# Optimization experiments

Measured on AMD Instinct MI355X. Metric: run time of the kernel, lower is better.

Reference implementation:

```python
import jax, jax.numpy as jnp
import numpy as np

B, C, N, V, W = 2, 4, 224, 7, 256
EMB, H = 256, 4
TOKEN_DIM = C * N           # 896
HF = int(C * 2.66)          # 10 (GDFN hidden features)
EPS_LN = 1e-6


def _dwconv3(x, w):
    # depthwise 3x3, padding=1; x:[B,Ch,Hh,Ww], w:[Ch,1,3,3]
    return jax.lax.conv_general_dilated(
        x, w, window_strides=(1, 1), padding='SAME',
        feature_group_count=x.shape[1],
        dimension_numbers=('NCHW', 'OIHW', 'NCHW'))


def _layernorm_c(x, g, b):
    # LayerNorm over channel dim (NCHW), eps=1e-6
    m = jnp.mean(x, axis=1, keepdims=True)
    v = jnp.mean((x - m) ** 2, axis=1, keepdims=True)
    return (x - m) / jnp.sqrt(v + EPS_LN) * g[None, :, None, None] + b[None, :, None, None]


def setup_inputs() -> dict:
    key = jax.random.key(0)
    ks = jax.random.split(key, 12)
    s = 0.02
    return {
        'buffer':     jax.random.normal(ks[0], (B, C, N, V, W), jnp.float32),
        'w_in':       jax.random.normal(ks[1], (EMB, TOKEN_DIM), jnp.float32) * s,
        'temperature': jnp.ones((1, H, 1, 1), jnp.float32),
        'ln1_g':      jnp.ones((EMB,), jnp.float32),
        'ln1_b':      jnp.zeros((EMB,), jnp.float32),
        'w_qkv':      jax.random.normal(ks[2], (3 * EMB, EMB), jnp.float32) * s,
        'w_qkv_dw':   jax.random.normal(ks[3], (3 * EMB, 1, 3, 3), jnp.float32) * s,
        'w_proj':     jax.random.normal(ks[4], (TOKEN_DIM, EMB), jnp.float32) * s,
        'w_attca':    jax.random.normal(ks[5], (2 * H, H), jnp.float32) * s,
        'ln2_g':      jnp.ones((C,), jnp.float32),
        'ln2_b':      jnp.zeros((C,), jnp.float32),
        'w_pin':      jax.random.normal(ks[6], (2 * HF, C), jnp.float32) * s,
        'w_dw':       jax.random.normal(ks[7], (2 * HF, 1, 3, 3), jnp.float32) * s,
        'w_pout':     jax.random.normal(ks[8], (C, HF), jnp.float32) * s,
    }


def reference(buffer, w_in, temperature, ln1_g, ln1_b, w_qkv, w_qkv_dw,
              w_proj, w_attca, ln2_g, ln2_b, w_pin, w_dw, w_pout):
    S = V * W
    d = EMB // H
    # b c n v w -> b (v w) (c n)
    x_tok = buffer.transpose(0, 3, 4, 1, 2).reshape(B, S, C * N)
    # b c n v w -> (b n) c v w
    x_res = buffer.transpose(0, 2, 1, 3, 4).reshape(B * N, C, V, W)

    x_tok = jnp.einsum('bsk,ek->bse', x_tok, w_in)                  # linear_in
    x = x_tok.reshape(B, V, W, EMB).transpose(0, 3, 1, 2)           # b emb v w
    x_norm = _layernorm_c(x, ln1_g, ln1_b)

    qkv = jnp.einsum('bchw,oc->bohw', x_norm, w_qkv)                # 1x1 conv
    qkv = _dwconv3(qkv, w_qkv_dw)
    q, k, v_ = jnp.split(qkv, 3, axis=1)

    def heads(t):  # b (h d) v w -> b h (v w) d
        return t.reshape(B, H, d, S).transpose(0, 1, 3, 2)
    q, k, v_ = heads(q), heads(k), heads(v_)

    # F.normalize(dim=-1), eps=1e-12
    q = q / jnp.maximum(jnp.linalg.norm(q, axis=-1, keepdims=True), 1e-12)
    k = k / jnp.maximum(jnp.linalg.norm(k, axis=-1, keepdims=True), 1e-12)

    attn_logits = jnp.einsum('bhid,bhjd->bhij', q, k) * temperature
    attn0 = jax.nn.softmax(attn_logits, axis=-1)
    attn1 = jnp.maximum(attn_logits, 0.0) ** 2
    attn1 = jax.nn.gelu(attn1, approximate=False) * attn1
    x_att = jnp.einsum('bhij,oh->boij', attn1, w_attca)             # 1x1 conv over heads
    scale, shift = jnp.split(x_att, 2, axis=1)
    attn = attn0 * (1.0 + scale) + shift

    out = jnp.einsum('bhij,bhjd->bhid', attn, v_)
    out = out.transpose(0, 1, 3, 2).reshape(B, EMB, V, W)           # b (h d) v w
    out = jnp.einsum('bchw,oc->bohw', out, w_proj)                  # proj to token_dim
    out = out.reshape(B, C, N, V, W).transpose(0, 2, 1, 3, 4).reshape(B * N, C, V, W)

    x2 = x_res + out
    epi = _layernorm_c(x2, ln2_g, ln2_b)
    # GDFN
    h_ = jnp.einsum('bchw,oc->bohw', epi, w_pin)
    h_ = _dwconv3(h_, w_dw)
    h1, h2 = jnp.split(h_, 2, axis=1)
    h_ = jax.nn.gelu(h1, approximate=False) * h2
    epi = jnp.einsum('bchw,oc->bohw', h_, w_pout)
    epi = x2 + epi

    return epi.reshape(B, N, C, V, W).transpose(0, 2, 1, 3, 4)      # b c n v w
```

## Files before the change

### kernel.cpp

```cpp
#include <hip/hip_runtime.h>
#include <math.h>

#define B_ 2
#define C_ 4
#define N_ 224
#define V_ 7
#define W_ 256
#define S_ 1792
#define EMB_ 256
#define H_ 4
#define D_ 64
#define TOK_ 896
#define HF_ 10
#define JC_ 4
#define JRANGE_ (S_ / JC_)
#define JSTEPS_ (JRANGE_ / 32)

typedef __attribute__((ext_vector_type(8))) short short8;
typedef __attribute__((ext_vector_type(4))) float f32x4;

#define MFMA16(a, b, c) __builtin_amdgcn_mfma_f32_16x16x32_bf16(a, b, c, 0, 0, 0)

__device__ inline short f2bf(float f) {
    union { float f; unsigned u; } x; x.f = f;
    unsigned u = x.u;
    unsigned r = (u + 0x7fffu + ((u >> 16) & 1u)) >> 16;
    return (short)r;
}
__device__ inline float bf2f(short s) {
    union { unsigned u; float f; } x;
    x.u = ((unsigned)(unsigned short)s) << 16;
    return x.f;
}

template<bool COLSUM, bool LNB, bool BBF>
__global__ __launch_bounds__(256) void gemm_kernel(
    const float* __restrict__ A, const void* __restrict__ Bv, float* __restrict__ Cm,
    int M, int N, int K, long b_bs, long c_bs,
    const float* __restrict__ csin, float* __restrict__ csout,
    const float* __restrict__ lg, const float* __restrict__ lb)
{
    const int bz = blockIdx.z;
    Cm += (long)bz * c_bs;
    const int m0 = blockIdx.y * 64, n0 = blockIdx.x * 128;
    __shared__ __align__(16) short As[64 * 32];
    __shared__ __align__(16) short Bs[128 * 32];
    const int t = threadIdx.x;
    const int lane = t & 63, wave = t >> 6;
    const int wr = wave >> 1, wc = wave & 1;
    const int col = lane & 15, grp = lane >> 4;
    const int arow = t >> 2, akc = (t & 3) * 8;
    const int bn = t & 127, bkc = (t >> 7) * 16;
    float mean = 0.f, rstd = 1.f;
    if (LNB) {
        float s = 0.f, q = 0.f;
        #pragma unroll
        for (int mb = 0; mb < 4; ++mb) {
            s += csin[((long)(bz * 4 + mb) * 2 + 0) * N + n0 + bn];
            q += csin[((long)(bz * 4 + mb) * 2 + 1) * N + n0 + bn];
        }
        mean = s * (1.f / 256.f);
        rstd = rsqrtf(q * (1.f / 256.f) - mean * mean + 1e-6f);
    }
    f32x4 acc[2][4];
    #pragma unroll
    for (int i = 0; i < 2; ++i)
        #pragma unroll
        for (int j = 0; j < 4; ++j) acc[i][j] = (f32x4){0.f, 0.f, 0.f, 0.f};
    for (int k0 = 0; k0 < K; k0 += 32) {
        {
            const float* ap = &A[(long)(m0 + arow) * K + k0 + akc];
            f32x4 a0 = *(const f32x4*)ap;
            f32x4 a1 = *(const f32x4*)(ap + 4);
            short8 av;
            av[0] = f2bf(a0[0]); av[1] = f2bf(a0[1]); av[2] = f2bf(a0[2]); av[3] = f2bf(a0[3]);
            av[4] = f2bf(a1[0]); av[5] = f2bf(a1[1]); av[6] = f2bf(a1[2]); av[7] = f2bf(a1[3]);
            int abyte = (arow << 6) + (akc << 1);
            *(short8*)((char*)As + (abyte ^ ((arow & 7) << 4))) = av;
        }
        {
            short8 b0, b1;
            if (BBF) {
                const short* Bp = (const short*)Bv + (long)bz * b_bs;
                #pragma unroll
                for (int j = 0; j < 8; ++j) {
                    b0[j] = Bp[(long)(k0 + bkc + j) * N + n0 + bn];
                    b1[j] = Bp[(long)(k0 + bkc + 8 + j) * N + n0 + bn];
                }
            } else {
                const float* Bp = (const float*)Bv + (long)bz * b_bs;
                #pragma unroll
                for (int j = 0; j < 16; ++j) {
                    float v = Bp[(long)(k0 + bkc + j) * N + n0 + bn];
                    if (LNB) v = fmaf((v - mean) * rstd, lg[k0 + bkc + j], lb[k0 + bkc + j]);
                    if (j < 8) b0[j] = f2bf(v); else b1[j - 8] = f2bf(v);
                }
            }
            int bbyte = (bn << 6) + (bkc << 1);
            *(short8*)((char*)Bs + ((bbyte) ^ ((bn & 7) << 4))) = b0;
            *(short8*)((char*)Bs + ((bbyte + 16) ^ ((bn & 7) << 4))) = b1;
        }
        __syncthreads();
        short8 af[2], bfv[4];
        #pragma unroll
        for (int mm = 0; mm < 2; ++mm) {
            int r = wr * 32 + mm * 16 + col;
            af[mm] = *(const short8*)((const char*)As + (((r << 6) + (grp << 4)) ^ ((r & 7) << 4)));
        }
        #pragma unroll
        for (int nn = 0; nn < 4; ++nn) {
            int r = wc * 64 + nn * 16 + col;
            bfv[nn] = *(const short8*)((const char*)Bs + (((r << 6) + (grp << 4)) ^ ((r & 7) << 4)));
        }
        #pragma unroll
        for (int mm = 0; mm < 2; ++mm)
            #pragma unroll
            for (int nn = 0; nn < 4; ++nn)
                acc[mm][nn] = MFMA16(af[mm], bfv[nn], acc[mm][nn]);
        __syncthreads();
    }
    #pragma unroll
    for (int mm = 0; mm < 2; ++mm)
        #pragma unroll
        for (int nn = 0; nn < 4; ++nn)
            #pragma unroll
            for (int r = 0; r < 4; ++r)
                Cm[(long)(m0 + wr * 32 + mm * 16 + grp * 4 + r) * N
                   + n0 + wc * 64 + nn * 16 + col] = acc[mm][nn][r];
    if (COLSUM) {
        float* red = (float*)As;
        #pragma unroll
        for (int nn = 0; nn < 4; ++nn) {
            float s = 0.f, q = 0.f;
            #pragma unroll
            for (int mm = 0; mm < 2; ++mm)
                #pragma unroll
                for (int r = 0; r < 4; ++r) { float v = acc[mm][nn][r]; s += v; q += v * v; }
            s += __shfl_xor(s, 16, 64); s += __shfl_xor(s, 32, 64);
            q += __shfl_xor(q, 16, 64); q += __shfl_xor(q, 32, 64);
            if (lane < 16) {
                int cidx = wc * 64 + nn * 16 + col;
                red[(wr * 128 + cidx) * 2]     = s;
                red[(wr * 128 + cidx) * 2 + 1] = q;
            }
        }
        __syncthreads();
        if (wave < 2 && lane < 16) {
            #pragma unroll
            for (int nn = 0; nn < 4; ++nn) {
                int cidx = wc * 64 + nn * 16 + col;
                float s = red[cidx * 2]     + red[(128 + cidx) * 2];
                float q = red[cidx * 2 + 1] + red[(128 + cidx) * 2 + 1];
                csout[((long)(bz * 4 + blockIdx.y) * 2 + 0) * N + n0 + cidx] = s;
                csout[((long)(bz * 4 + blockIdx.y) * 2 + 1) * N + n0 + cidx] = q;
            }
        }
    }
}

__global__ void dwconv3_kernel(const float* __restrict__ X, const float* __restrict__ Wt,
                               float* __restrict__ Y, short* __restrict__ vbf,
                               long total, int Ch)
{
    long idx = (long)blockIdx.x * blockDim.x + threadIdx.x;
    long stride = (long)gridDim.x * blockDim.x;
    for (; idx < total; idx += stride) {
        int w = (int)(idx % W_);
        long t = idx / W_;
        int h = (int)(t % V_); t /= V_;
        int ch = (int)(t % Ch);
        long img_ch = idx / ((long)V_ * W_);
        const float* wp = Wt + ch * 9;
        const float* xp = X + img_ch * (V_ * W_);
        float acc = 0.f;
        #pragma unroll
        for (int dy = -1; dy <= 1; ++dy) {
            int h2 = h + dy;
            if (h2 < 0 || h2 >= V_) continue;
            #pragma unroll
            for (int dx = -1; dx <= 1; ++dx) {
                int w2 = w + dx;
                if (w2 < 0 || w2 >= W_) continue;
                acc += xp[h2 * W_ + w2] * wp[(dy + 1) * 3 + (dx + 1)];
            }
        }
        Y[idx] = acc;
        if (vbf && ch >= 512) {
            int b = (int)(t / Ch);
            vbf[((long)b * 256 + (ch - 512)) * S_ + h * W_ + w] = f2bf(acc);
        }
    }
}

__global__ __launch_bounds__(256) void headnorm_kernel(
    const float* __restrict__ qkvd, const float* __restrict__ temp,
    short* __restrict__ qn, short* __restrict__ kn)
{
    int s0 = blockIdx.x * 64;
    int bh = blockIdx.y; int b = bh >> 2, h = bh & 3;
    int isq = blockIdx.z;
    int ch0 = b * 768 + (isq ? 0 : EMB_) + h * 64;
    short* dst = (isq ? qn : kn) + (long)bh * S_ * 64;
    __shared__ float tile[64][65];
    __shared__ float red[64][4];
    int t = threadIdx.x;
    int sl = t & 63, dg = t >> 6;
    float part = 0.f;
    for (int dd = 0; dd < 16; ++dd) {
        int d = dg * 16 + dd;
        float v = qkvd[(long)(ch0 + d) * S_ + s0 + sl];
        tile[sl][d] = v;
        part += v * v;
    }
    red[sl][dg] = part;
    __syncthreads();
    int d = t & 63, sg = t >> 6;
    float tmul = isq ? temp[h] : 1.f;
    for (int si = 0; si < 16; ++si) {
        int s = sg * 16 + si;
        float nrm = sqrtf(red[s][0] + red[s][1] + red[s][2] + red[s][3]);
        float scale = tmul / fmaxf(nrm, 1e-12f);
        dst[(long)(s0 + s) * 64 + d] = f2bf(tile[s][d] * scale);
    }
}

__global__ __launch_bounds__(256) void attn_kernel(
    const short* __restrict__ qn, const short* __restrict__ kn,
    const short* __restrict__ vbf, const float* __restrict__ wat,
    short* __restrict__ partY, float* __restrict__ partZ)
{
    const int h = threadIdx.x >> 6;
    const int lane = threadIdx.x & 63;
    const int col = lane & 15, grp = lane >> 4;
    const int itile = blockIdx.x;
    const int jc = blockIdx.y;
    const int b = blockIdx.z;
    const int ibase = itile * 16;
    const int bh = b * 4 + h;

    const short* qrow = qn + ((long)bh * S_ + ibase + col) * 64 + grp * 8;
    short8 qa0 = *(const short8*)qrow;
    short8 qa1 = *(const short8*)(qrow + 32);
    float wsc[4], wsh[4];
    #pragma unroll
    for (int hh = 0; hh < 4; ++hh) { wsc[hh] = wat[h * 4 + hh]; wsh[hh] = wat[(4 + h) * 4 + hh]; }

    __shared__ __align__(16) float exch[2][4][16][36];

    f32x4 y1[4], y2[4];
    #pragma unroll
    for (int dt = 0; dt < 4; ++dt) {
        y1[dt] = (f32x4){0.f, 0.f, 0.f, 0.f};
        y2[dt] = (f32x4){0.f, 0.f, 0.f, 0.f};
    }
    float z = 0.f;
    const short* kbase = kn + (long)bh * S_ * 64;
    const short* vbase = vbf + ((long)b * 256 + h * 64) * S_;
    const int joffA = (col & 3) + 8 * (col >> 2);

    for (int jt = 0; jt < JSTEPS_; ++jt) {
        const int jbase = jc * JRANGE_ + jt * 32;
        const int buf = jt & 1;
        f32x4 lf[2];
        __builtin_amdgcn_s_setprio(1);
        #pragma unroll
        for (int tt = 0; tt < 2; ++tt) {
            const short* krow = kbase + (long)(jbase + joffA + 4 * tt) * 64 + grp * 8;
            short8 ka0 = *(const short8*)krow;
            short8 ka1 = *(const short8*)(krow + 32);
            f32x4 a = (f32x4){0.f, 0.f, 0.f, 0.f};
            a = MFMA16(ka0, qa0, a);
            a = MFMA16(ka1, qa1, a);
            lf[tt] = a;
        }
        __builtin_amdgcn_s_setprio(0);
        f32x4 a1v[2];
        float ee[2][4];
        #pragma unroll
        for (int tt = 0; tt < 2; ++tt) {
            #pragma unroll
            for (int r = 0; r < 4; ++r) {
                float l = lf[tt][r];
                float rr = fmaxf(l, 0.f);
                float s1 = rr * rr;
                float u = fmaf(s1 * s1, 0.0713548162726f * s1, 1.59576912161f * s1);
                float sg = __builtin_amdgcn_rcpf(1.f + __expf(-u));
                a1v[tt][r] = s1 * sg * s1;
                ee[tt][r] = __expf(l);
            }
            *(f32x4*)&exch[buf][h][col][8 * grp + 4 * tt] = a1v[tt];
        }
        __syncthreads();
        short8 pa, pb;
        #pragma unroll
        for (int tt = 0; tt < 2; ++tt) {
            f32x4 scv = a1v[tt] * wsc[h];
            f32x4 shv = a1v[tt] * wsh[h];
            #pragma unroll
            for (int hh = 0; hh < 4; ++hh) {
                if (hh == h) continue;
                f32x4 o = *(const f32x4*)&exch[buf][hh][col][8 * grp + 4 * tt];
                scv += o * wsc[hh];
                shv += o * wsh[hh];
            }
            #pragma unroll
            for (int r = 0; r < 4; ++r) {
                float e = ee[tt][r];
                z += e;
                pa[tt * 4 + r] = f2bf(e * (1.f + scv[r]));
                pb[tt * 4 + r] = f2bf(shv[r]);
            }
        }
        __builtin_amdgcn_s_setprio(1);
        #pragma unroll
        for (int dt = 0; dt < 4; ++dt) {
            const short* vrow = vbase + (long)(dt * 16 + col) * S_ + jbase + grp * 8;
            short8 vb = *(const short8*)vrow;
            y1[dt] = MFMA16(pa, vb, y1[dt]);
            y2[dt] = MFMA16(pb, vb, y2[dt]);
        }
        __builtin_amdgcn_s_setprio(0);
    }

    z += __shfl_xor(z, 16, 64);
    z += __shfl_xor(z, 32, 64);
    if (grp == 0)
        partZ[((long)(jc * 2 + b) * 4 + h) * S_ + ibase + col] = z;

    float* tb = &exch[0][h][0][0];
    long ybase = ((((long)jc * 2 + b) * 4 + h) * 2) * 64 * S_;
    for (int acc = 0; acc < 2; ++acc) {
        #pragma unroll
        for (int dt = 0; dt < 4; ++dt) {
            f32x4 y = acc ? y2[dt] : y1[dt];
            #pragma unroll
            for (int r = 0; r < 4; ++r) tb[(grp * 4 + r) * 17 + col] = y[r];
            #pragma unroll
            for (int p = 0; p < 4; ++p) {
                float val = tb[col * 17 + p * 4 + grp];
                partY[ybase + ((long)acc * 64 + dt * 16 + p * 4 + grp) * S_ + ibase + col] = f2bf(val);
            }
        }
    }
}

__global__ __launch_bounds__(256) void combine_kernel(
    const short* __restrict__ partY, const float* __restrict__ partZ,
    short* __restrict__ outav)
{
    int idx = blockIdx.x * 256 + threadIdx.x;
    int i = idx % S_;
    int t = idx / S_;
    int d = t & 63; t >>= 6;
    int h = t & 3; int b = t >> 2;
    float y1 = 0.f, y2 = 0.f, z = 0.f;
    #pragma unroll
    for (int jc = 0; jc < JC_; ++jc) {
        long base = ((((long)jc * 2 + b) * 4 + h) * 2) * 64 * S_;
        y1 += bf2f(partY[base + (long)d * S_ + i]);
        y2 += bf2f(partY[base + (long)(64 + d) * S_ + i]);
        z  += partZ[((long)(jc * 2 + b) * 4 + h) * S_ + i];
    }
    outav[((long)b * 256 + h * 64 + d) * S_ + i] = f2bf(y1 / z + y2);
}

__global__ __launch_bounds__(256) void resid_pin_kernel(
    const float* __restrict__ buffer, const float* __restrict__ proj,
    const float* __restrict__ g2, const float* __restrict__ b2,
    const float* __restrict__ w_pin,
    float* __restrict__ x2, short* __restrict__ hbuf)
{
    int s = blockIdx.x * 256 + threadIdx.x;
    int bn = blockIdx.y;
    int b = bn / N_, n = bn % N_;
    float v[4];
    float sum = 0.f;
    #pragma unroll
    for (int c = 0; c < 4; ++c) {
        float xr = buffer[((long)(b * 4 + c) * N_ + n) * S_ + s];
        float pr = proj[((long)b * TOK_ + c * N_ + n) * S_ + s];
        v[c] = xr + pr;
        x2[((long)bn * 4 + c) * S_ + s] = v[c];
        sum += v[c];
    }
    float mean = sum * 0.25f;
    float var = 0.f;
    #pragma unroll
    for (int c = 0; c < 4; ++c) { float dd = v[c] - mean; var += dd * dd; }
    var *= 0.25f;
    float inv = rsqrtf(var + 1e-6f);
    float e[4];
    #pragma unroll
    for (int c = 0; c < 4; ++c) e[c] = (v[c] - mean) * inv * g2[c] + b2[c];
    for (int o = 0; o < 2 * HF_; ++o) {
        float a = 0.f;
        #pragma unroll
        for (int c = 0; c < 4; ++c) a += w_pin[o * 4 + c] * e[c];
        hbuf[((long)bn * (2 * HF_) + o) * S_ + s] = f2bf(a);
    }
}

__global__ __launch_bounds__(448) void gdfn_kernel(
    const short* __restrict__ hbuf, const float* __restrict__ w_dw,
    const float* __restrict__ w_pout, const float* __restrict__ x2,
    float* __restrict__ out)
{
    int xt = blockIdx.x;
    int bn = blockIdx.y;
    int b = bn / N_, n = bn % N_;
    int x0 = xt * 64;
    __shared__ float tile[20][7][66];
    int tid = threadIdx.x;
    for (int idx = tid; idx < 20 * 7 * 66; idx += 448) {
        int ch = idx / (7 * 66); int rem = idx % (7 * 66);
        int y = rem / 66; int xx = rem % 66;
        int gx = x0 + xx - 1;
        float v = 0.f;
        if (gx >= 0 && gx < W_) v = bf2f(hbuf[((long)bn * 20 + ch) * S_ + y * W_ + gx]);
        tile[ch][y][xx] = v;
    }
    __syncthreads();
    int y = tid / 64, x = tid & 63;
    float hd[20];
    #pragma unroll
    for (int ch = 0; ch < 20; ++ch) {
        const float* wp = w_dw + ch * 9;
        float acc = 0.f;
        #pragma unroll
        for (int dy = -1; dy <= 1; ++dy) {
            int yy = y + dy;
            if (yy < 0 || yy >= V_) continue;
            #pragma unroll
            for (int dx = -1; dx <= 1; ++dx)
                acc += tile[ch][yy][x + 1 + dx] * wp[(dy + 1) * 3 + (dx + 1)];
        }
        hd[ch] = acc;
    }
    float g[HF_];
    #pragma unroll
    for (int f = 0; f < HF_; ++f) {
        float h1 = hd[f];
        g[f] = 0.5f * h1 * (1.f + erff(h1 * 0.70710678118654752f)) * hd[HF_ + f];
    }
    int s = y * W_ + x0 + x;
    #pragma unroll
    for (int c = 0; c < 4; ++c) {
        float a = 0.f;
        #pragma unroll
        for (int f = 0; f < HF_; ++f) a += w_pout[c * HF_ + f] * g[f];
        out[((long)(b * 4 + c) * N_ + n) * S_ + s] = x2[((long)bn * 4 + c) * S_ + s] + a;
    }
}

extern "C" void kernel_launch(void* const* d_in, const int* in_sizes, int n_in,
                              void* d_out, int out_size, void* d_ws, size_t ws_size,
                              hipStream_t stream)
{
    const float* buffer = (const float*)d_in[0];
    const float* w_in   = (const float*)d_in[1];
    const float* temp   = (const float*)d_in[2];
    const float* ln1_g  = (const float*)d_in[3];
    const float* ln1_b  = (const float*)d_in[4];
    const float* w_qkv  = (const float*)d_in[5];
    const float* w_qkv_dw = (const float*)d_in[6];
    const float* w_proj = (const float*)d_in[7];
    const float* w_attca = (const float*)d_in[8];
    const float* ln2_g  = (const float*)d_in[9];
    const float* ln2_b  = (const float*)d_in[10];
    const float* w_pin  = (const float*)d_in[11];
    const float* w_dw   = (const float*)d_in[12];
    const float* w_pout = (const float*)d_in[13];
    float* out = (float*)d_out;

    float* ws = (float*)d_ws;
    float* qkvd    = ws;
    short* qn      = (short*)(ws + 2752512);
    short* kn      = (short*)(ws + 3211264);
    short* vbf     = (short*)(ws + 3670016);
    short* partY   = (short*)(ws + 4128768);
    float* partZ   = ws + 7798784;
    short* outav   = (short*)(ws + 7856128);
    float* xw      = ws + 8314880;
    float* colsum  = ws + 9232384;
    float* qkv     = ws + 9261056;
    float* outproj = ws + 12013568;
    float* x2      = ws + 15224832;
    short* hbuf    = (short*)(ws + 18436096);

    gemm_kernel<true, false, false><<<dim3(14, 4, 2), 256, 0, stream>>>(
        w_in, buffer, xw, EMB_, S_, TOK_, (long)TOK_ * S_, (long)EMB_ * S_,
        nullptr, colsum, nullptr, nullptr);

    gemm_kernel<false, true, false><<<dim3(14, 12, 2), 256, 0, stream>>>(
        w_qkv, xw, qkv, 3 * EMB_, S_, EMB_, (long)EMB_ * S_, (long)3 * EMB_ * S_,
        colsum, nullptr, ln1_g, ln1_b);

    {
        long total = (long)B_ * 3 * EMB_ * S_;
        dwconv3_kernel<<<(int)((total + 255) / 256), 256, 0, stream>>>(
            qkv, w_qkv_dw, qkvd, vbf, total, 3 * EMB_);
    }

    headnorm_kernel<<<dim3(28, 8, 2), 256, 0, stream>>>(qkvd, temp, qn, kn);

    attn_kernel<<<dim3(112, JC_, B_), 256, 0, stream>>>(qn, kn, vbf, w_attca, partY, partZ);

    combine_kernel<<<3584, 256, 0, stream>>>(partY, partZ, outav);

    gemm_kernel<false, false, true><<<dim3(14, 14, 2), 256, 0, stream>>>(
        w_proj, outav, outproj, TOK_, S_, EMB_, (long)EMB_ * S_, (long)TOK_ * S_,
        nullptr, nullptr, nullptr, nullptr);

    resid_pin_kernel<<<dim3(7, B_ * N_), 256, 0, stream>>>(
        buffer, outproj, ln2_g, ln2_b, w_pin, x2, hbuf);

    gdfn_kernel<<<dim3(4, B_ * N_), 448, 0, stream>>>(hbuf, w_dw, w_pout, x2, out);
}
```

Measured before the change: 217.2 us.

## Fuse dwconv into head-norm prep, fuse epilogue kernels, double attention j-splits

Merges the qkv depthwise conv with q/k L2 normalisation and the v bf16 conversion into one qkprep kernel, which removes the fp32 qkvd intermediate. It also merges the residual+LN2+pin and GDFN kernels into one epilogue that rebuilds x2 on the fly, dropping the x2 and hbuf buffers. Attention now uses twice as many j-chunks, and it swaps the double-buffered exchange and setprio hints for a single buffer with an extra barrier. The trade-offs are recomputed halo columns in the epilogue, more partial results to combine, and an extra __syncthreads on every attention step.

```diff
diff --git a/kernel.cpp b/kernel.cpp
--- a/kernel.cpp
+++ b/kernel.cpp
@@ -12,7 +12,7 @@
 #define D_ 64
 #define TOK_ 896
 #define HF_ 10
-#define JC_ 4
+#define JC_ 8
 #define JRANGE_ (S_ / JC_)
 #define JSTEPS_ (JRANGE_ / 32)
 
@@ -158,64 +158,61 @@
     }
 }
 
-__global__ void dwconv3_kernel(const float* __restrict__ X, const float* __restrict__ Wt,
-                               float* __restrict__ Y, short* __restrict__ vbf,
-                               long total, int Ch)
-{
-    long idx = (long)blockIdx.x * blockDim.x + threadIdx.x;
-    long stride = (long)gridDim.x * blockDim.x;
-    for (; idx < total; idx += stride) {
-        int w = (int)(idx % W_);
-        long t = idx / W_;
-        int h = (int)(t % V_); t /= V_;
-        int ch = (int)(t % Ch);
-        long img_ch = idx / ((long)V_ * W_);
-        const float* wp = Wt + ch * 9;
-        const float* xp = X + img_ch * (V_ * W_);
+__global__ __launch_bounds__(256) void qkprep_kernel(
+    const float* __restrict__ qkv, const float* __restrict__ temp,
+    const float* __restrict__ w_qkv_dw,
+    short* __restrict__ qn, short* __restrict__ kn, short* __restrict__ vbf)
+{
+    const int s0 = blockIdx.x * 64;
+    const int y  = s0 >> 8;
+    const int x0 = s0 & 255;
+    const int bh = blockIdx.y; const int b = bh >> 2, h = bh & 3;
+    const int mode = blockIdx.z;
+    const int wchbase = (mode == 0 ? 256 : (mode == 1 ? 0 : 512)) + h * 64;
+    const int chbase = b * 768 + wchbase;
+
+    int t = threadIdx.x;
+    int sl = t & 63, dg = t >> 6;
+    int x = x0 + sl;
+    float dval[16];
+    float part = 0.f;
+    #pragma unroll
+    for (int dd = 0; dd < 16; ++dd) {
+        int ch = dg * 16 + dd;
+        const float* xp = qkv + (long)(chbase + ch) * S_;
+        const float* wp = w_qkv_dw + (long)(wchbase + ch) * 9;
         float acc = 0.f;
         #pragma unroll
         for (int dy = -1; dy <= 1; ++dy) {
-            int h2 = h + dy;
-            if (h2 < 0 || h2 >= V_) continue;
+            int yy = y + dy;
+            if (yy < 0 || yy >= V_) continue;
+            const float* rp = xp + yy * W_;
             #pragma unroll
             for (int dx = -1; dx <= 1; ++dx) {
-                int w2 = w + dx;
-                if (w2 < 0 || w2 >= W_) continue;
-                acc += xp[h2 * W_ + w2] * wp[(dy + 1) * 3 + (dx + 1)];
-            }
-        }
-        Y[idx] = acc;
-        if (vbf && ch >= 512) {
-            int b = (int)(t / Ch);
-            vbf[((long)b * 256 + (ch - 512)) * S_ + h * W_ + w] = f2bf(acc);
-        }
-    }
-}
-
-__global__ __launch_bounds__(256) void headnorm_kernel(
-    const float* __restrict__ qkvd, const float* __restrict__ temp,
-    short* __restrict__ qn, short* __restrict__ kn)
-{
-    int s0 = blockIdx.x * 64;
-    int bh = blockIdx.y; int b = bh >> 2, h = bh & 3;
-    int isq = blockIdx.z;
-    int ch0 = b * 768 + (isq ? 0 : EMB_) + h * 64;
-    short* dst = (isq ? qn : kn) + (long)bh * S_ * 64;
+                int xx2 = x + dx;
+                if (xx2 < 0 || xx2 >= W_) continue;
+                acc += rp[xx2] * wp[(dy + 1) * 3 + dx + 1];
+            }
+        }
+        dval[dd] = acc;
+        part += acc * acc;
+    }
+    if (mode == 2) {
+        short* dst = vbf + ((long)b * 256 + h * 64) * S_;
+        #pragma unroll
+        for (int dd = 0; dd < 16; ++dd)
+            dst[(long)(dg * 16 + dd) * S_ + s0 + sl] = f2bf(dval[dd]);
+        return;
+    }
     __shared__ float tile[64][65];
     __shared__ float red[64][4];
-    int t = threadIdx.x;
-    int sl = t & 63, dg = t >> 6;
-    float part = 0.f;
-    for (int dd = 0; dd < 16; ++dd) {
-        int d = dg * 16 + dd;
-        float v = qkvd[(long)(ch0 + d) * S_ + s0 + sl];
-        tile[sl][d] = v;
-        part += v * v;
-    }
+    #pragma unroll
+    for (int dd = 0; dd < 16; ++dd) tile[sl][dg * 16 + dd] = dval[dd];
     red[sl][dg] = part;
     __syncthreads();
     int d = t & 63, sg = t >> 6;
-    float tmul = isq ? temp[h] : 1.f;
+    float tmul = (mode == 1) ? temp[h] : 1.f;
+    short* dst = (mode == 1 ? qn : kn) + (long)bh * S_ * 64;
     for (int si = 0; si < 16; ++si) {
         int s = sg * 16 + si;
         float nrm = sqrtf(red[s][0] + red[s][1] + red[s][2] + red[s][3]);
@@ -245,7 +242,7 @@
     #pragma unroll
     for (int hh = 0; hh < 4; ++hh) { wsc[hh] = wat[h * 4 + hh]; wsh[hh] = wat[(4 + h) * 4 + hh]; }
 
-    __shared__ __align__(16) float exch[2][4][16][36];
+    __shared__ __align__(16) float exch[4][16][36];
 
     f32x4 y1[4], y2[4];
     #pragma unroll
@@ -259,10 +256,8 @@
     const int joffA = (col & 3) + 8 * (col >> 2);
 
     for (int jt = 0; jt < JSTEPS_; ++jt) {
-        const int jbase = jc * JRANGE_ + jt * 32;
-        const int buf = jt & 1;
+        int jbase = jc * JRANGE_ + jt * 32;
         f32x4 lf[2];
-        __builtin_amdgcn_s_setprio(1);
         #pragma unroll
         for (int tt = 0; tt < 2; ++tt) {
             const short* krow = kbase + (long)(jbase + joffA + 4 * tt) * 64 + grp * 8;
@@ -273,7 +268,6 @@
             a = MFMA16(ka1, qa1, a);
             lf[tt] = a;
         }
-        __builtin_amdgcn_s_setprio(0);
         f32x4 a1v[2];
         float ee[2][4];
         #pragma unroll
@@ -288,7 +282,7 @@
                 a1v[tt][r] = s1 * sg * s1;
                 ee[tt][r] = __expf(l);
             }
-            *(f32x4*)&exch[buf][h][col][8 * grp + 4 * tt] = a1v[tt];
+            *(f32x4*)&exch[h][col][8 * grp + 4 * tt] = a1v[tt];
         }
         __syncthreads();
         short8 pa, pb;
@@ -299,7 +293,7 @@
             #pragma unroll
             for (int hh = 0; hh < 4; ++hh) {
                 if (hh == h) continue;
-                f32x4 o = *(const f32x4*)&exch[buf][hh][col][8 * grp + 4 * tt];
+                f32x4 o = *(const f32x4*)&exch[hh][col][8 * grp + 4 * tt];
                 scv += o * wsc[hh];
                 shv += o * wsh[hh];
             }
@@ -311,7 +305,7 @@
                 pb[tt * 4 + r] = f2bf(shv[r]);
             }
         }
-        __builtin_amdgcn_s_setprio(1);
+        __syncthreads();
         #pragma unroll
         for (int dt = 0; dt < 4; ++dt) {
             const short* vrow = vbase + (long)(dt * 16 + col) * S_ + jbase + grp * 8;
@@ -319,7 +313,6 @@
             y1[dt] = MFMA16(pa, vb, y1[dt]);
             y2[dt] = MFMA16(pb, vb, y2[dt]);
         }
-        __builtin_amdgcn_s_setprio(0);
     }
 
     z += __shfl_xor(z, 16, 64);
@@ -327,7 +320,8 @@
     if (grp == 0)
         partZ[((long)(jc * 2 + b) * 4 + h) * S_ + ibase + col] = z;
 
-    float* tb = &exch[0][h][0][0];
+    __syncthreads();
+    float* tb = &exch[h][0][0];
     long ybase = ((((long)jc * 2 + b) * 4 + h) * 2) * 64 * S_;
     for (int acc = 0; acc < 2; ++acc) {
         #pragma unroll
@@ -364,91 +358,84 @@
     outav[((long)b * 256 + h * 64 + d) * S_ + i] = f2bf(y1 / z + y2);
 }
 
-__global__ __launch_bounds__(256) void resid_pin_kernel(
+__global__ __launch_bounds__(448) void epi_kernel(
     const float* __restrict__ buffer, const float* __restrict__ proj,
     const float* __restrict__ g2, const float* __restrict__ b2,
-    const float* __restrict__ w_pin,
-    float* __restrict__ x2, short* __restrict__ hbuf)
-{
-    int s = blockIdx.x * 256 + threadIdx.x;
-    int bn = blockIdx.y;
-    int b = bn / N_, n = bn % N_;
-    float v[4];
-    float sum = 0.f;
-    #pragma unroll
-    for (int c = 0; c < 4; ++c) {
-        float xr = buffer[((long)(b * 4 + c) * N_ + n) * S_ + s];
-        float pr = proj[((long)b * TOK_ + c * N_ + n) * S_ + s];
-        v[c] = xr + pr;
-        x2[((long)bn * 4 + c) * S_ + s] = v[c];
-        sum += v[c];
-    }
-    float mean = sum * 0.25f;
-    float var = 0.f;
-    #pragma unroll
-    for (int c = 0; c < 4; ++c) { float dd = v[c] - mean; var += dd * dd; }
-    var *= 0.25f;
-    float inv = rsqrtf(var + 1e-6f);
-    float e[4];
-    #pragma unroll
-    for (int c = 0; c < 4; ++c) e[c] = (v[c] - mean) * inv * g2[c] + b2[c];
-    for (int o = 0; o < 2 * HF_; ++o) {
-        float a = 0.f;
-        #pragma unroll
-        for (int c = 0; c < 4; ++c) a += w_pin[o * 4 + c] * e[c];
-        hbuf[((long)bn * (2 * HF_) + o) * S_ + s] = f2bf(a);
-    }
-}
-
-__global__ __launch_bounds__(448) void gdfn_kernel(
-    const short* __restrict__ hbuf, const float* __restrict__ w_dw,
-    const float* __restrict__ w_pout, const float* __restrict__ x2,
-    float* __restrict__ out)
-{
-    int xt = blockIdx.x;
-    int bn = blockIdx.y;
-    int b = bn / N_, n = bn % N_;
-    int x0 = xt * 64;
-    __shared__ float tile[20][7][66];
-    int tid = threadIdx.x;
-    for (int idx = tid; idx < 20 * 7 * 66; idx += 448) {
-        int ch = idx / (7 * 66); int rem = idx % (7 * 66);
-        int y = rem / 66; int xx = rem % 66;
+    const float* __restrict__ w_pin, const float* __restrict__ w_dw,
+    const float* __restrict__ w_pout, float* __restrict__ out)
+{
+    const int half = blockIdx.x;
+    const int bn = blockIdx.y;
+    const int b = bn / N_, n = bn % N_;
+    const int x0 = half * 128;
+    __shared__ short hl[20][7][130];
+    const int tid = threadIdx.x;
+    for (int idx = tid; idx < 7 * 130; idx += 448) {
+        int yy = idx / 130, xx = idx % 130;
         int gx = x0 + xx - 1;
-        float v = 0.f;
-        if (gx >= 0 && gx < W_) v = bf2f(hbuf[((long)bn * 20 + ch) * S_ + y * W_ + gx]);
-        tile[ch][y][xx] = v;
+        if (gx < 0 || gx >= W_) {
+            #pragma unroll
+            for (int o = 0; o < 20; ++o) hl[o][yy][xx] = 0;
+        } else {
+            int s = yy * W_ + gx;
+            float v[4]; float sum = 0.f;
+            #pragma unroll
+            for (int c = 0; c < 4; ++c) {
+                float xr = buffer[((long)(b * 4 + c) * N_ + n) * S_ + s];
+                float pr = proj[((long)b * TOK_ + c * N_ + n) * S_ + s];
+                v[c] = xr + pr; sum += v[c];
+            }
+            float mean = sum * 0.25f;
+            float var = 0.f;
+            #pragma unroll
+            for (int c = 0; c < 4; ++c) { float dd2 = v[c] - mean; var += dd2 * dd2; }
+            float inv = rsqrtf(var * 0.25f + 1e-6f);
+            float e[4];
+            #pragma unroll
+            for (int c = 0; c < 4; ++c) e[c] = (v[c] - mean) * inv * g2[c] + b2[c];
+            #pragma unroll
+            for (int o = 0; o < 20; ++o) {
+                float a = 0.f;
+                #pragma unroll
+                for (int c = 0; c < 4; ++c) a += w_pin[o * 4 + c] * e[c];
+                hl[o][yy][xx] = f2bf(a);
+            }
+        }
     }
     __syncthreads();
-    int y = tid / 64, x = tid & 63;
-    float hd[20];
-    #pragma unroll
-    for (int ch = 0; ch < 20; ++ch) {
-        const float* wp = w_dw + ch * 9;
-        float acc = 0.f;
-        #pragma unroll
-        for (int dy = -1; dy <= 1; ++dy) {
-            int yy = y + dy;
-            if (yy < 0 || yy >= V_) continue;
-            #pragma unroll
-            for (int dx = -1; dx <= 1; ++dx)
-                acc += tile[ch][yy][x + 1 + dx] * wp[(dy + 1) * 3 + (dx + 1)];
-        }
-        hd[ch] = acc;
-    }
-    float g[HF_];
-    #pragma unroll
-    for (int f = 0; f < HF_; ++f) {
-        float h1 = hd[f];
-        g[f] = 0.5f * h1 * (1.f + erff(h1 * 0.70710678118654752f)) * hd[HF_ + f];
-    }
-    int s = y * W_ + x0 + x;
-    #pragma unroll
-    for (int c = 0; c < 4; ++c) {
-        float a = 0.f;
-        #pragma unroll
-        for (int f = 0; f < HF_; ++f) a += w_pout[c * HF_ + f] * g[f];
-        out[((long)(b * 4 + c) * N_ + n) * S_ + s] = x2[((long)bn * 4 + c) * S_ + s] + a;
+    for (int pos = tid; pos < 7 * 128; pos += 448) {
+        int yy = pos / 128, xl = pos % 128;
+        int s = yy * W_ + x0 + xl;
+        float hd[20];
+        #pragma unroll
+        for (int ch = 0; ch < 20; ++ch) {
+            const float* wp = w_dw + ch * 9;
+            float acc = 0.f;
+            #pragma unroll
+            for (int dy = -1; dy <= 1; ++dy) {
+                int y2 = yy + dy;
+                if (y2 < 0 || y2 >= V_) continue;
+                #pragma unroll
+                for (int dx = -1; dx <= 1; ++dx)
+                    acc += bf2f(hl[ch][y2][xl + 1 + dx]) * wp[(dy + 1) * 3 + dx + 1];
+            }
+            hd[ch] = acc;
+        }
+        float g[HF_];
+        #pragma unroll
+        for (int f = 0; f < HF_; ++f) {
+            float h1 = hd[f];
+            g[f] = 0.5f * h1 * (1.f + erff(h1 * 0.70710678118654752f)) * hd[HF_ + f];
+        }
+        #pragma unroll
+        for (int c = 0; c < 4; ++c) {
+            float a = 0.f;
+            #pragma unroll
+            for (int f = 0; f < HF_; ++f) a += w_pout[c * HF_ + f] * g[f];
+            float xr = buffer[((long)(b * 4 + c) * N_ + n) * S_ + s];
+            float pr = proj[((long)b * TOK_ + c * N_ + n) * S_ + s];
+            out[((long)(b * 4 + c) * N_ + n) * S_ + s] = xr + pr + a;
+        }
     }
 }
 
@@ -473,19 +460,16 @@
     float* out = (float*)d_out;
 
     float* ws = (float*)d_ws;
-    float* qkvd    = ws;
+    float* qkv     = ws;
     short* qn      = (short*)(ws + 2752512);
     short* kn      = (short*)(ws + 3211264);
     short* vbf     = (short*)(ws + 3670016);
     short* partY   = (short*)(ws + 4128768);
-    float* partZ   = ws + 7798784;
-    short* outav   = (short*)(ws + 7856128);
-    float* xw      = ws + 8314880;
-    float* colsum  = ws + 9232384;
-    float* qkv     = ws + 9261056;
-    float* outproj = ws + 12013568;
-    float* x2      = ws + 15224832;
-    short* hbuf    = (short*)(ws + 18436096);
+    float* partZ   = ws + 11468800;
+    short* outav   = (short*)(ws + 11583488);
+    float* xw      = ws + 12042240;
+    float* colsum  = ws + 12959744;
+    float* outproj = ws + 12988416;
 
     gemm_kernel<true, false, false><<<dim3(14, 4, 2), 256, 0, stream>>>(
         w_in, buffer, xw, EMB_, S_, TOK_, (long)TOK_ * S_, (long)EMB_ * S_,
@@ -495,13 +479,8 @@
         w_qkv, xw, qkv, 3 * EMB_, S_, EMB_, (long)EMB_ * S_, (long)3 * EMB_ * S_,
         colsum, nullptr, ln1_g, ln1_b);
 
-    {
-        long total = (long)B_ * 3 * EMB_ * S_;
-        dwconv3_kernel<<<(int)((total + 255) / 256), 256, 0, stream>>>(
-            qkv, w_qkv_dw, qkvd, vbf, total, 3 * EMB_);
-    }
-
-    headnorm_kernel<<<dim3(28, 8, 2), 256, 0, stream>>>(qkvd, temp, qn, kn);
+    qkprep_kernel<<<dim3(28, 8, 3), 256, 0, stream>>>(
+        qkv, temp, w_qkv_dw, qn, kn, vbf);
 
     attn_kernel<<<dim3(112, JC_, B_), 256, 0, stream>>>(qn, kn, vbf, w_attca, partY, partZ);
 
@@ -511,8 +490,6 @@
         w_proj, outav, outproj, TOK_, S_, EMB_, (long)EMB_ * S_, (long)TOK_ * S_,
         nullptr, nullptr, nullptr, nullptr);
 
-    resid_pin_kernel<<<dim3(7, B_ * N_), 256, 0, stream>>>(
-        buffer, outproj, ln2_g, ln2_b, w_pin, x2, hbuf);
-
-    gdfn_kernel<<<dim3(4, B_ * N_), 448, 0, stream>>>(hbuf, w_dw, w_pout, x2, out);
-}
+    epi_kernel<<<dim3(2, B_ * N_), 448, 0, stream>>>(
+        buffer, outproj, ln2_g, ln2_b, w_pin, w_dw, w_pout, out);
+}
```

After: 261.4 us. +20.3%, slower.
